# Optimization experiments

Measured on AMD Instinct MI355X. Metric: run time of the kernel, lower is better.

## Reference

```python
import jax, jax.numpy as jnp
import numpy as np

R_MAX = 32
S_MAX = 2
TOKEN_Z = 128
B, N = 1, 1024
NUM_POS = 2 * R_MAX + 2      # 66 bins for residue-index distance
NUM_TOK = 2 * R_MAX + 2      # 66 bins for token-index distance
NUM_CHAIN = 2 * S_MAX + 2    # 6 bins for chain (symmetry) distance
D_IN = NUM_POS + NUM_TOK + 1 + NUM_CHAIN  # 139 = 4*(r_max+1) + 2*(s_max+1) + 1


def setup_inputs() -> dict:
    key = jax.random.key(0)
    ks = jax.random.split(key, 6)
    asym_id = jax.random.randint(ks[0], (B, N), 0, 4)
    residue_index = jax.random.randint(ks[1], (B, N), 0, 512)
    entity_id = jax.random.randint(ks[2], (B, N), 0, 2)
    token_index = jax.random.randint(ks[3], (B, N), 0, 1024)
    sym_id = jax.random.randint(ks[4], (B, N), 0, 4)
    W = jax.random.normal(ks[5], (D_IN, TOKEN_Z), dtype=jnp.float32) / np.sqrt(D_IN).astype(np.float32)
    return {
        'asym_id': asym_id,
        'residue_index': residue_index,
        'entity_id': entity_id,
        'token_index': token_index,
        'sym_id': sym_id,
        'W': W,
    }


def _bin_indices(asym_id, residue_index, token_index, sym_id):
    """Compute the per-pair bin index for each of the three one-hot features."""
    same_chain = asym_id[:, :, None] == asym_id[:, None, :]            # [B,N,N]
    same_residue = residue_index[:, :, None] == residue_index[:, None, :]

    d_res = jnp.clip(residue_index[:, :, None] - residue_index[:, None, :] + R_MAX, 0, 2 * R_MAX)
    d_res = jnp.where(same_chain, d_res, 2 * R_MAX + 1)

    d_tok = jnp.clip(token_index[:, :, None] - token_index[:, None, :] + R_MAX, 0, 2 * R_MAX)
    d_tok = jnp.where(same_chain & same_residue, d_tok, 2 * R_MAX + 1)

    d_chain = jnp.clip(sym_id[:, :, None] - sym_id[:, None, :] + S_MAX, 0, 2 * S_MAX)
    d_chain = jnp.where(same_chain, 2 * S_MAX + 1, d_chain)
    return d_res, d_tok, d_chain


def reference(asym_id, residue_index, entity_id, token_index, sym_id, W):
    # Fused gather-sum: one_hot(d) @ W_block == W_block[d], so the concat of
    # one-hots followed by LinearNoBias equals a sum of 3 row-gathers from W
    # plus the same-entity flag times one W row. Identical math to the
    # original, without materializing the [B,N,N,139] one-hot/concat tensor.
    d_res, d_tok, d_chain = _bin_indices(asym_id, residue_index, token_index, sym_id)
    same_entity = (entity_id[:, :, None] == entity_id[:, None, :]).astype(W.dtype)  # [B,N,N]

    W_pos = W[:NUM_POS]                                  # [66, Z]
    W_tok = W[NUM_POS:NUM_POS + NUM_TOK]                 # [66, Z]
    w_ent = W[NUM_POS + NUM_TOK]                         # [Z]
    W_chain = W[NUM_POS + NUM_TOK + 1:]                  # [6, Z]

    p = W_pos[d_res] + W_tok[d_tok] + W_chain[d_chain] + same_entity[..., None] * w_ent
    return p  # [B, N, N, token_z]
```

## Files before the change

### kernel.cpp

```cpp
#include <hip/hip_runtime.h>


#define N_TOK   1024
#define R_MAX   32
#define S_MAX   2
#define ROW_POS   0
#define ROW_TOK   66
#define ROW_ENT   132
#define ROW_CHAIN 133

__global__ __launch_bounds__(256) void relpos_kernel(
    const int*   __restrict__ asym_id,
    const int*   __restrict__ residue_index,
    const int*   __restrict__ entity_id,
    const int*   __restrict__ token_index,
    const int*   __restrict__ sym_id,
    const float* __restrict__ W,
    float*       __restrict__ out)
{
    const long long tid = (long long)blockIdx.x * blockDim.x + threadIdx.x;
    const int pair = (int)(tid >> 5);
    const int slot = (int)(tid & 31);
    if (pair >= N_TOK * N_TOK) return;

    const int i = pair >> 10;
    const int j = pair & (N_TOK - 1);

    const int ai = asym_id[i],       aj = asym_id[j];
    const int ri = residue_index[i], rj = residue_index[j];
    const int ti = token_index[i],   tj = token_index[j];
    const int si = sym_id[i],        sj = sym_id[j];
    const int ei = entity_id[i],     ej = entity_id[j];

    const bool same_chain = (ai == aj);
    const bool same_res   = (ri == rj);

    int d_res = min(max(ri - rj + R_MAX, 0), 2 * R_MAX);
    if (!same_chain) d_res = 2 * R_MAX + 1;

    int d_tok = min(max(ti - tj + R_MAX, 0), 2 * R_MAX);
    if (!(same_chain && same_res)) d_tok = 2 * R_MAX + 1;

    int d_chain = same_chain ? (2 * S_MAX + 1)
                             : min(max(si - sj + S_MAX, 0), 2 * S_MAX);

    const float4* __restrict__ W4 = (const float4*)W;
    const float4 a = W4[(ROW_POS   + d_res)   * 32 + slot];
    const float4 b = W4[(ROW_TOK   + d_tok)   * 32 + slot];
    const float4 c = W4[(ROW_CHAIN + d_chain) * 32 + slot];

    float4 r;
    r.x = a.x + b.x + c.x;
    r.y = a.y + b.y + c.y;
    r.z = a.z + b.z + c.z;
    r.w = a.w + b.w + c.w;

    if (ei == ej) {
        const float4 e = W4[ROW_ENT * 32 + slot];
        r.x += e.x; r.y += e.y; r.z += e.z; r.w += e.w;
    }

    ((float4*)out)[(long long)pair * 32 + slot] = r;
}

extern "C" void kernel_launch(void* const* d_in, const int* in_sizes, int n_in,
                              void* d_out, int out_size, void* d_ws, size_t ws_size,
                              hipStream_t stream) {
    const int*   asym_id       = (const int*)d_in[0];
    const int*   residue_index = (const int*)d_in[1];
    const int*   entity_id     = (const int*)d_in[2];
    const int*   token_index   = (const int*)d_in[3];
    const int*   sym_id        = (const int*)d_in[4];
    const float* W             = (const float*)d_in[5];
    float*       out           = (float*)d_out;

    const long long total_threads = (long long)N_TOK * N_TOK * 32;
    const int block = 256;
    const int grid  = (int)((total_threads + block - 1) / block);

    relpos_kernel<<<grid, block, 0, stream>>>(
        asym_id, residue_index, entity_id, token_index, sym_id, W, out);
}
```

Measured before the change: 117.1 us.

## Compute pair bin indices once per pair in shared memory, loop over pairs per thread

Each block now handles 64 pairs (one row i, 64 columns j). The first 64 threads compute the packed bin indices into shared memory, then all 256 threads each write 8 float4 outputs in a loop. This removes the redundant per-lane index loads and arithmetic (previously every one of 32 lanes per pair recomputed them) and cuts the grid size by 8x, at the cost of a __syncthreads and a serial index-compute phase. The entity row is loaded once and applied with a multiply instead of a branch.

```diff
diff --git a/kernel.cpp b/kernel.cpp
--- a/kernel.cpp
+++ b/kernel.cpp
@@ -18,49 +18,66 @@
     const float* __restrict__ W,
     float*       __restrict__ out)
 {
-    const long long tid = (long long)blockIdx.x * blockDim.x + threadIdx.x;
-    const int pair = (int)(tid >> 5);
-    const int slot = (int)(tid & 31);
-    if (pair >= N_TOK * N_TOK) return;
+    __shared__ int s_idx[64];
 
-    const int i = pair >> 10;
-    const int j = pair & (N_TOK - 1);
+    const int tid = threadIdx.x;
+    const int i   = blockIdx.x >> 4;
+    const int j0  = (blockIdx.x & 15) << 6;
 
-    const int ai = asym_id[i],       aj = asym_id[j];
-    const int ri = residue_index[i], rj = residue_index[j];
-    const int ti = token_index[i],   tj = token_index[j];
-    const int si = sym_id[i],        sj = sym_id[j];
-    const int ei = entity_id[i],     ej = entity_id[j];
+    if (tid < 64) {
+        const int j  = j0 + tid;
+        const int ai = asym_id[i],       aj = asym_id[j];
+        const int ri = residue_index[i], rj = residue_index[j];
+        const int ti = token_index[i],   tj = token_index[j];
+        const int si = sym_id[i],        sj = sym_id[j];
+        const int ei = entity_id[i],     ej = entity_id[j];
 
-    const bool same_chain = (ai == aj);
-    const bool same_res   = (ri == rj);
+        const bool same_chain = (ai == aj);
+        const bool same_res   = (ri == rj);
 
-    int d_res = min(max(ri - rj + R_MAX, 0), 2 * R_MAX);
-    if (!same_chain) d_res = 2 * R_MAX + 1;
+        int d_res = min(max(ri - rj + R_MAX, 0), 2 * R_MAX);
+        if (!same_chain) d_res = 2 * R_MAX + 1;
 
-    int d_tok = min(max(ti - tj + R_MAX, 0), 2 * R_MAX);
-    if (!(same_chain && same_res)) d_tok = 2 * R_MAX + 1;
+        int d_tok = min(max(ti - tj + R_MAX, 0), 2 * R_MAX);
+        if (!(same_chain && same_res)) d_tok = 2 * R_MAX + 1;
 
-    int d_chain = same_chain ? (2 * S_MAX + 1)
-                             : min(max(si - sj + S_MAX, 0), 2 * S_MAX);
+        const int d_chain = same_chain ? (2 * S_MAX + 1)
+                                       : min(max(si - sj + S_MAX, 0), 2 * S_MAX);
+        const int ent = (ei == ej) ? 1 : 0;
+
+        s_idx[tid] = d_res | (d_tok << 7) | (d_chain << 14) | (ent << 17);
+    }
+    __syncthreads();
+
+    const int slot    = tid & 31;
+    const int plocal0 = tid >> 5;
 
     const float4* __restrict__ W4 = (const float4*)W;
-    const float4 a = W4[(ROW_POS   + d_res)   * 32 + slot];
-    const float4 b = W4[(ROW_TOK   + d_tok)   * 32 + slot];
-    const float4 c = W4[(ROW_CHAIN + d_chain) * 32 + slot];
+    const float4 e = W4[ROW_ENT * 32 + slot];
 
-    float4 r;
-    r.x = a.x + b.x + c.x;
-    r.y = a.y + b.y + c.y;
-    r.z = a.z + b.z + c.z;
-    r.w = a.w + b.w + c.w;
+    float4* __restrict__ outp = (float4*)out + ((long long)blockIdx.x << 11);
 
-    if (ei == ej) {
-        const float4 e = W4[ROW_ENT * 32 + slot];
-        r.x += e.x; r.y += e.y; r.z += e.z; r.w += e.w;
+    #pragma unroll
+    for (int iter = 0; iter < 8; ++iter) {
+        const int pl      = plocal0 + iter * 8;
+        const int packed  = s_idx[pl];
+        const int d_res   =  packed        & 127;
+        const int d_tok   = (packed >> 7)  & 127;
+        const int d_chain = (packed >> 14) & 7;
+        const float m     = (packed & (1 << 17)) ? 1.0f : 0.0f;
+
+        const float4 a = W4[(ROW_POS   + d_res)   * 32 + slot];
+        const float4 b = W4[(ROW_TOK   + d_tok)   * 32 + slot];
+        const float4 c = W4[(ROW_CHAIN + d_chain) * 32 + slot];
+
+        float4 r;
+        r.x = a.x + b.x + c.x + m * e.x;
+        r.y = a.y + b.y + c.y + m * e.y;
+        r.z = a.z + b.z + c.z + m * e.z;
+        r.w = a.w + b.w + c.w + m * e.w;
+
+        outp[pl * 32 + slot] = r;
     }
-
-    ((float4*)out)[(long long)pair * 32 + slot] = r;
 }
 
 extern "C" void kernel_launch(void* const* d_in, const int* in_sizes, int n_in,
@@ -74,9 +91,8 @@
     const float* W             = (const float*)d_in[5];
     float*       out           = (float*)d_out;
 
-    const long long total_threads = (long long)N_TOK * N_TOK * 32;
+    const int grid  = (N_TOK * N_TOK) / 64;
     const int block = 256;
-    const int grid  = (int)((total_threads + block - 1) / block);
 
     relpos_kernel<<<grid, block, 0, stream>>>(
         asym_id, residue_index, entity_id, token_index, sym_id, W, out);
```

New measurement: 106.4 us. 1.1x faster.
